# Kernel tuning notes

Hardware: AMD Instinct MI355X
Metric: run time of the kernel (lower is better)

## Reference

```python
import jax, jax.numpy as jnp
import numpy as np

D_MODEL = 512
N_HEADS = 8
D_HEAD = D_MODEL // N_HEADS
EPS = 1e-5


def layer_norm(x, g, b):
    mu = jnp.mean(x, axis=-1, keepdims=True)
    var = jnp.mean(jnp.square(x - mu), axis=-1, keepdims=True)
    return (x - mu) * jax.lax.rsqrt(var + EPS) * g + b


def setup_inputs() -> dict:
    key = jax.random.key(0)
    ks = jax.random.split(key, 8)
    B, L, D = 2, 4096, D_MODEL
    x = jax.random.normal(ks[0], (B, L, D), dtype=jnp.float32)
    # monotonically increasing event timestamps (hours)
    timestamps = jnp.sort(jax.random.uniform(ks[1], (B, L), dtype=jnp.float32) * 1000.0, axis=-1)
    mask = jnp.ones((B, L), dtype=jnp.float32)
    s = 0.02
    return {
        "x": x,
        "timestamps": timestamps,
        "mask": mask,
        "ln1_g": jnp.ones((D,), jnp.float32),
        "ln1_b": jnp.zeros((D,), jnp.float32),
        "w_qkv": jax.random.normal(ks[2], (3 * D, D), jnp.float32) * s,
        "w_out": jax.random.normal(ks[3], (D, D), jnp.float32) * s,
        "decay_rate": jnp.ones((N_HEADS,), jnp.float32) * 0.01,
        "ln2_g": jnp.ones((D,), jnp.float32),
        "ln2_b": jnp.zeros((D,), jnp.float32),
        "w_ff1": jax.random.normal(ks[4], (4 * D, D), jnp.float32) * s,
        "w_ff2": jax.random.normal(ks[5], (D, 4 * D), jnp.float32) * s,
    }


def reference(x, timestamps, mask, ln1_g, ln1_b, w_qkv, w_out, decay_rate, ln2_g, ln2_b, w_ff1, w_ff2):
    B, L, D = x.shape
    H, dh = N_HEADS, D_HEAD
    scale = dh ** (-0.5)

    xn = layer_norm(x, ln1_g, ln1_b)
    qkv = (xn @ w_qkv.T).reshape(B, L, 3, H, dh).transpose(2, 0, 3, 1, 4)  # [3,B,H,L,dh]
    q, k, v = qkv[0], qkv[1], qkv[2]

    attn = jnp.einsum("bhid,bhjd->bhij", q, k) * scale  # [B,H,L,L]

    # temporal-decay bias
    t_diff = jnp.abs(timestamps[:, None, :, None] - timestamps[:, None, None, :]) / 24.0  # [B,1,L,L]
    decay = jax.nn.softplus(decay_rate)[None, :, None, None]  # [1,H,1,1]
    attn = attn - decay * t_diff

    # causal mask
    causal = jnp.triu(jnp.ones((L, L), dtype=bool), k=1)
    attn = jnp.where(causal[None, None], -jnp.inf, attn)

    # padding mask over keys
    pad = (mask == 0)[:, None, None, :]  # [B,1,1,L]
    attn = jnp.where(pad, -jnp.inf, attn)

    attn = jax.nn.softmax(attn, axis=-1)
    out = jnp.einsum("bhij,bhjd->bhid", attn, v).transpose(0, 2, 1, 3).reshape(B, L, D)

    x = x + out @ w_out.T
    h = layer_norm(x, ln2_g, ln2_b)
    x = x + jax.nn.silu(h @ w_ff1.T) @ w_ff2.T
    return x
```

## Files before the change

### kernel.cpp

```cpp
#include <hip/hip_runtime.h>
#include <hip/hip_bf16.h>
#include <cmath>


#define L_SEQ 4096
#define D_MODEL 512
#define N_HEADS 8
#define D_HEAD 64
#define QKV_LD 1536

typedef __attribute__((ext_vector_type(8))) short bf16x8;
typedef __attribute__((ext_vector_type(4))) float f32x4;
typedef __attribute__((ext_vector_type(4))) unsigned u32x4;

__device__ __forceinline__ __hip_bfloat16 f2bf(float v) { return __float2bfloat16(v); }

__device__ __forceinline__ float exp2_raw(float x) {
  float r;
  asm("v_exp_f32 %0, %1" : "=v"(r) : "v"(x));
  return r;
}

__device__ __forceinline__ void gl_lds16(const __hip_bfloat16* g, __hip_bfloat16* l) {
  __builtin_amdgcn_global_load_lds((__attribute__((address_space(1))) void*)g,
                                   (__attribute__((address_space(3))) void*)l, 16, 0, 0);
}

__global__ __launch_bounds__(256) void cvt4b_kernel(const float* __restrict__ s0, __hip_bfloat16* __restrict__ d0,
                                                    const float* __restrict__ s1, __hip_bfloat16* __restrict__ d1,
                                                    const float* __restrict__ s2, __hip_bfloat16* __restrict__ d2,
                                                    const float* __restrict__ s3, __hip_bfloat16* __restrict__ d3,
                                                    const float* __restrict__ ts,
                                                    const float* __restrict__ mask,
                                                    const float* __restrict__ decay_rate,
                                                    float* __restrict__ biasH) {
  const int i = blockIdx.x * 256 + threadIdx.x;
  if (i < 786432) {
    const float* s;
    __hip_bfloat16* d;
    int off;
    if (i < 196608) { s = s0; d = d0; off = i; }
    else if (i < 262144) { s = s1; d = d1; off = i - 196608; }
    else if (i < 524288) { s = s2; d = d2; off = i - 262144; }
    else { s = s3; d = d3; off = i - 524288; }
    const float4 v = ((const float4*)s)[off];
    d[4 * off + 0] = f2bf(v.x);
    d[4 * off + 1] = f2bf(v.y);
    d[4 * off + 2] = f2bf(v.z);
    d[4 * off + 3] = f2bf(v.w);
  } else {
    const int idx = i - 786432;
    const int col = idx & 4095;
    const int h = (idx >> 12) & 7;
    const int b = idx >> 15;
    const float LOG2E = 1.4426950408889634f;
    const float dfac = log1pf(expf(decay_rate[h])) * (1.0f / 24.0f) * LOG2E;
    const float m = mask[b * 4096 + col];
    biasH[idx] = dfac * ts[b * 4096 + col] + (m != 0.f ? 0.f : -1e30f);
  }
}

__global__ __launch_bounds__(256) void ln_kernel(const float* __restrict__ x,
                                                 const float* __restrict__ g,
                                                 const float* __restrict__ b,
                                                 __hip_bfloat16* __restrict__ out) {
  const int row = blockIdx.x;
  const int t = threadIdx.x;
  const float* xr = x + (size_t)row * D_MODEL;
  float v0 = xr[t];
  float v1 = xr[t + 256];
  float s = v0 + v1;
  float qq = v0 * v0 + v1 * v1;
  for (int off = 32; off > 0; off >>= 1) {
    s += __shfl_xor(s, off);
    qq += __shfl_xor(qq, off);
  }
  __shared__ float red[8];
  const int wid = t >> 6;
  if ((t & 63) == 0) { red[wid] = s; red[4 + wid] = qq; }
  __syncthreads();
  s = red[0] + red[1] + red[2] + red[3];
  qq = red[4] + red[5] + red[6] + red[7];
  const float mu = s * (1.0f / 512.0f);
  const float var = fmaxf(qq * (1.0f / 512.0f) - mu * mu, 0.0f);
  const float rstd = rsqrtf(var + 1e-5f);
  __hip_bfloat16* orow = out + (size_t)row * D_MODEL;
  orow[t] = f2bf((v0 - mu) * rstd * g[t] + b[t]);
  orow[t + 256] = f2bf((v1 - mu) * rstd * g[t + 256] + b[t + 256]);
}

__global__ __launch_bounds__(256) void vtrans_kernel(const __hip_bfloat16* __restrict__ qkv,
                                                     __hip_bfloat16* __restrict__ vt) {
  const int gid = blockIdx.x * 256 + threadIdx.x;
  const int l = gid & 4095;
  const int bg = gid >> 12;
  const int b = bg >> 6, g = bg & 63;
  const int h = g >> 3, dg = (g & 7) * 8;
  const __hip_bfloat16* src = qkv + (size_t)(b * L_SEQ + l) * QKV_LD + 1024 + h * 64 + dg;
  bf16x8 v = *(const bf16x8*)src;
  const int kin = l & 63;
  const int sl = (kin & 0x23) | ((kin & 0x10) >> 2) | ((kin & 0x0c) << 1);
  const size_t dbase = (size_t)((b * 8 + h) * 64 + dg) * L_SEQ + (l & ~63) + sl;
  for (int j = 0; j < 8; j++)
    vt[dbase + (size_t)j * L_SEQ] = ((const __hip_bfloat16*)&v)[j];
}

template <int EPI>
__global__ __launch_bounds__(256) void gemm_kernel(const __hip_bfloat16* __restrict__ A,
                                                   const __hip_bfloat16* __restrict__ B,
                                                   int M, int N, int K,
                                                   const float* __restrict__ aux,
                                                   void* __restrict__ C) {
  __shared__ __align__(16) __hip_bfloat16 As[2][128 * 32];
  __shared__ __align__(16) __hip_bfloat16 Bs[2][128 * 32];
  const int tid = threadIdx.x;
  const int lane = tid & 63, w = tid >> 6;
  const int m0 = blockIdx.y * 128, n0 = blockIdx.x * 128;
  const int wm = (w >> 1) * 64, wn = (w & 1) * 64;
  const int r = lane & 15, q = lane >> 4;

  f32x4 acc[4][4];
  const f32x4 zz = {0.f, 0.f, 0.f, 0.f};
  for (int i = 0; i < 4; i++)
    for (int j = 0; j < 4; j++) acc[i][j] = zz;

  const int c0 = tid, c1 = 256 + tid;
  const int row0 = c0 >> 2, kb0 = (c0 & 3) * 8;
  const int row1 = c1 >> 2, kb1 = (c1 & 3) * 8;

#define GEMM_STAGE(k0, buf)                                                     \
  do {                                                                          \
    gl_lds16(A + (size_t)(m0 + row0) * K + ((k0) + kb0), &As[buf][c0 * 8]);     \
    gl_lds16(B + (size_t)(n0 + row0) * K + ((k0) + kb0), &Bs[buf][c0 * 8]);     \
    gl_lds16(A + (size_t)(m0 + row1) * K + ((k0) + kb1), &As[buf][c1 * 8]);     \
    gl_lds16(B + (size_t)(n0 + row1) * K + ((k0) + kb1), &Bs[buf][c1 * 8]);     \
  } while (0)

  GEMM_STAGE(0, 0);
  const int niter = K >> 5;
  for (int it = 0; it < niter; it++) {
    const int cur = it & 1;
    if (it + 1 < niter) {
      GEMM_STAGE((it + 1) << 5, cur ^ 1);
      asm volatile("s_waitcnt vmcnt(4)" ::: "memory");
    } else {
      asm volatile("s_waitcnt vmcnt(0)" ::: "memory");
    }
    __builtin_amdgcn_s_barrier();
    bf16x8 af[4], bfr[4];
    for (int mi = 0; mi < 4; mi++)
      af[mi] = *(const bf16x8*)(&As[cur][(wm + mi * 16 + r) * 32 + q * 8]);
    for (int ni = 0; ni < 4; ni++)
      bfr[ni] = *(const bf16x8*)(&Bs[cur][(wn + ni * 16 + r) * 32 + q * 8]);
    for (int mi = 0; mi < 4; mi++)
      for (int ni = 0; ni < 4; ni++)
        acc[mi][ni] = __builtin_amdgcn_mfma_f32_16x16x32_bf16(af[mi], bfr[ni], acc[mi][ni], 0, 0, 0);
    __builtin_amdgcn_s_barrier();
  }
#undef GEMM_STAGE

  for (int mi = 0; mi < 4; mi++)
    for (int ni = 0; ni < 4; ni++)
      for (int j = 0; j < 4; j++) {
        const int gm = m0 + wm + mi * 16 + q * 4 + j;
        const int gn = n0 + wn + ni * 16 + r;
        float v = acc[mi][ni][j];
        const size_t idx = (size_t)gm * N + gn;
        if (EPI == 0) {
          ((__hip_bfloat16*)C)[idx] = f2bf(v);
        } else {
          v = v / (1.0f + expf(-v));
          ((__hip_bfloat16*)C)[idx] = f2bf(v);
        }
      }
}

__global__ __launch_bounds__(256) void gemm_res64_kernel(const __hip_bfloat16* __restrict__ A,
                                                         const __hip_bfloat16* __restrict__ B,
                                                         int M, int N, int K,
                                                         const float* __restrict__ aux,
                                                         float* __restrict__ C) {
  __shared__ __align__(16) __hip_bfloat16 As[2][64 * 32];
  __shared__ __align__(16) __hip_bfloat16 Bs[2][128 * 32];
  const int tid = threadIdx.x;
  const int lane = tid & 63, w = tid >> 6;
  const int m0 = blockIdx.y * 64, n0 = blockIdx.x * 128;
  const int wm = (w >> 1) * 32, wn = (w & 1) * 64;
  const int r = lane & 15, q = lane >> 4;

  f32x4 acc[2][4];
  const f32x4 zz = {0.f, 0.f, 0.f, 0.f};
  for (int i = 0; i < 2; i++)
    for (int j = 0; j < 4; j++) acc[i][j] = zz;

  const int rowA = tid >> 2, kbA = (tid & 3) * 8;
  const int c0 = tid, c1 = 256 + tid;
  const int rowB0 = c0 >> 2, kb0 = (c0 & 3) * 8;
  const int rowB1 = c1 >> 2, kb1 = (c1 & 3) * 8;

#define GEMM_STAGE64(k0, buf)                                                    \
  do {                                                                           \
    gl_lds16(A + (size_t)(m0 + rowA) * K + ((k0) + kbA), &As[buf][tid * 8]);     \
    gl_lds16(B + (size_t)(n0 + rowB0) * K + ((k0) + kb0), &Bs[buf][c0 * 8]);     \
    gl_lds16(B + (size_t)(n0 + rowB1) * K + ((k0) + kb1), &Bs[buf][c1 * 8]);     \
  } while (0)

  GEMM_STAGE64(0, 0);
  const int niter = K >> 5;
  for (int it = 0; it < niter; it++) {
    const int cur = it & 1;
    if (it + 1 < niter) {
      GEMM_STAGE64((it + 1) << 5, cur ^ 1);
      asm volatile("s_waitcnt vmcnt(3)" ::: "memory");
    } else {
      asm volatile("s_waitcnt vmcnt(0)" ::: "memory");
    }
    __builtin_amdgcn_s_barrier();
    bf16x8 af[2], bfr[4];
    for (int mi = 0; mi < 2; mi++)
      af[mi] = *(const bf16x8*)(&As[cur][(wm + mi * 16 + r) * 32 + q * 8]);
    for (int ni = 0; ni < 4; ni++)
      bfr[ni] = *(const bf16x8*)(&Bs[cur][(wn + ni * 16 + r) * 32 + q * 8]);
    for (int mi = 0; mi < 2; mi++)
      for (int ni = 0; ni < 4; ni++)
        acc[mi][ni] = __builtin_amdgcn_mfma_f32_16x16x32_bf16(af[mi], bfr[ni], acc[mi][ni], 0, 0, 0);
    __builtin_amdgcn_s_barrier();
  }
#undef GEMM_STAGE64

  for (int mi = 0; mi < 2; mi++)
    for (int ni = 0; ni < 4; ni++)
      for (int j = 0; j < 4; j++) {
        const int gm = m0 + wm + mi * 16 + q * 4 + j;
        const int gn = n0 + wn + ni * 16 + r;
        const size_t idx = (size_t)gm * N + gn;
        C[idx] = acc[mi][ni][j] + aux[idx];
      }
}

__device__ __forceinline__ void stage_kv128(int w, int lane, int key0,
                                            const __hip_bfloat16* __restrict__ Kg,
                                            const __hip_bfloat16* __restrict__ Vg,
                                            __hip_bfloat16* Ks, __hip_bfloat16* Vs) {
  const int krow_in = lane >> 3;
  const int kcs = (lane & 7) ^ krow_in;
  const int vrow_in = lane >> 4;
  const int vch = lane & 15;
#pragma unroll
  for (int ii = 0; ii < 2; ii++) {
    const int i = w * 2 + ii;
    const int krow = i * 8 + krow_in;
    gl_lds16(Kg + (size_t)(key0 + krow) * QKV_LD + kcs * 8, Ks + i * 512 + lane * 8);
    const int vrow = i * 4 + vrow_in;
    const int vcs = vch ^ (vrow & 7);
    gl_lds16(Vg + (size_t)vrow * L_SEQ + key0 + vcs * 8, Vs + i * 512 + lane * 8);
  }
}

template <bool CAUSAL>
__device__ __forceinline__ void attn_tile128(int key0, int lw0, int r, int q,
                                             const __hip_bfloat16* Ks,
                                             const __hip_bfloat16* Vs,
                                             const float* biasLds,
                                             float scale2,
                                             const bf16x8& qf0, const bf16x8& qf1,
                                             const bf16x8& onesf,
                                             f32x4* o, f32x4& ls) {
  const int r7 = r & 7;
  const f32x4 zz = {0.f, 0.f, 0.f, 0.f};
  f32x4 bias4[8];
#pragma unroll
  for (int hc = 0; hc < 8; hc++)
    bias4[hc] = *(const f32x4*)(biasLds + key0 + hc * 16 + q * 4);
  f32x4 s[8];
  __builtin_amdgcn_s_setprio(1);
#pragma unroll
  for (int hc = 0; hc < 8; hc++) {
    const __hip_bfloat16* kr = Ks + (hc * 16 + r) * 64;
    bf16x8 k0 = *(const bf16x8*)(kr + ((q ^ r7) * 8));
    bf16x8 k1 = *(const bf16x8*)(kr + (((q + 4) ^ r7) * 8));
    f32x4 a = zz;
    a = __builtin_amdgcn_mfma_f32_16x16x32_bf16(k0, qf0, a, 0, 0, 0);
    a = __builtin_amdgcn_mfma_f32_16x16x32_bf16(k1, qf1, a, 0, 0, 0);
    s[hc] = a;
  }
  __builtin_amdgcn_s_setprio(0);
  float p[8][4];
#pragma unroll
  for (int hc = 0; hc < 8; hc++)
#pragma unroll
    for (int j = 0; j < 4; j++) {
      float pv = exp2_raw(fmaf(s[hc][j], scale2, bias4[hc][j]));
      if (CAUSAL) pv = (key0 + hc * 16 + q * 4 + j <= lw0 + r) ? pv : 0.f;
      p[hc][j] = pv;
    }
  bf16x8 pa[4];
#pragma unroll
  for (int kc = 0; kc < 4; kc++) {
    u32x4 pw;
    unsigned w0, w1, w2, w3;
    asm("v_cvt_pk_bf16_f32 %0, %1, %2" : "=v"(w0) : "v"(p[2 * kc][0]), "v"(p[2 * kc][1]));
    asm("v_cvt_pk_bf16_f32 %0, %1, %2" : "=v"(w1) : "v"(p[2 * kc][2]), "v"(p[2 * kc][3]));
    asm("v_cvt_pk_bf16_f32 %0, %1, %2" : "=v"(w2) : "v"(p[2 * kc + 1][0]), "v"(p[2 * kc + 1][1]));
    asm("v_cvt_pk_bf16_f32 %0, %1, %2" : "=v"(w3) : "v"(p[2 * kc + 1][2]), "v"(p[2 * kc + 1][3]));
    pw[0] = w0; pw[1] = w1; pw[2] = w2; pw[3] = w3;
    pa[kc] = *(bf16x8*)&pw;
  }
  __builtin_amdgcn_s_setprio(1);
#pragma unroll
  for (int kc = 0; kc < 4; kc++) {
#pragma unroll
    for (int c = 0; c < 4; c++) {
      const __hip_bfloat16* vr = Vs + (c * 16 + r) * 128 + (((kc * 4 + q) ^ r7) * 8);
      bf16x8 vf = *(const bf16x8*)vr;
      o[c] = __builtin_amdgcn_mfma_f32_16x16x32_bf16(pa[kc], vf, o[c], 0, 0, 0);
    }
    ls = __builtin_amdgcn_mfma_f32_16x16x32_bf16(pa[kc], onesf, ls, 0, 0, 0);
  }
  __builtin_amdgcn_s_setprio(0);
}

__global__ __launch_bounds__(512, 4) void attn_kernel(const __hip_bfloat16* __restrict__ qkv,
                                                      const __hip_bfloat16* __restrict__ vt,
                                                      const float* __restrict__ biasH,
                                                      __hip_bfloat16* __restrict__ out) {
  const int blk = blockIdx.x;
  const int bh = blk & 15;
  const int pr = blk >> 4;
  const int b = bh >> 3, h = bh & 7;
  const int tid = threadIdx.x, lane = tid & 63, w = tid >> 6;
  const int grp = w >> 2, wg = w & 3;
  const int qi = grp ? (63 - pr) : pr;
  const int l0 = qi * 64;
  const int lw0 = l0 + wg * 16;
  const int r = lane & 15, q = lane >> 4;

  __shared__ __align__(16) __hip_bfloat16 Ksm[2][128 * 64];
  __shared__ __align__(16) __hip_bfloat16 Vsm[2][64 * 128];
  __shared__ __align__(16) float biasLds[4096];

  const float LOG2E = 1.4426950408889634f;
  const float scale2 = 0.125f * LOG2E;

  const __hip_bfloat16* Kg = qkv + (size_t)b * L_SEQ * QKV_LD + 512 + h * 64;
  const __hip_bfloat16* Vg = vt + (size_t)bh * 64 * L_SEQ;
  const float* biasHp = biasH + (size_t)bh * L_SEQ;

  stage_kv128(w, lane, 0, Kg, Vg, Ksm[0], Vsm[0]);
#pragma unroll
  for (int ii = 0; ii < 2; ii++) {
    const int fo = (w * 2 + ii) * 256;
    gl_lds16((const __hip_bfloat16*)(biasHp + fo + lane * 4),
             (__hip_bfloat16*)(biasLds + fo + lane * 4));
  }

  bf16x8 qf0, qf1;
  {
    const __hip_bfloat16* qrow = qkv + (size_t)(b * L_SEQ + lw0 + r) * QKV_LD + h * 64 + q * 8;
    qf0 = *(const bf16x8*)qrow;
    qf1 = *(const bf16x8*)(qrow + 32);
  }

  const f32x4 zz = {0.f, 0.f, 0.f, 0.f};
  f32x4 o[4];
  for (int c = 0; c < 4; c++) o[c] = zz;
  f32x4 ls = zz;

  bf16x8 onesf;
  for (int i = 0; i < 8; i++) ((short*)&onesf)[i] = (short)0x3F80;

  const int ntA = (pr >> 1) + 1;
  const int ntB = ((63 - pr) >> 1) + 1;
  const int nt = grp ? ntB : ntA;

  for (int t = 0; t < ntB; t++) {
    const int cur = t & 1;
    if (t + 1 < ntB) {
      stage_kv128(w, lane, (t + 1) << 7, Kg, Vg, Ksm[cur ^ 1], Vsm[cur ^ 1]);
      asm volatile("s_waitcnt vmcnt(4)" ::: "memory");
    } else {
      asm volatile("s_waitcnt vmcnt(0)" ::: "memory");
    }
    __builtin_amdgcn_s_barrier();
    if (t < nt) {
      if (t == nt - 1)
        attn_tile128<true>(t << 7, lw0, r, q, Ksm[cur], Vsm[cur], biasLds, scale2, qf0, qf1,
                           onesf, o, ls);
      else
        attn_tile128<false>(t << 7, lw0, r, q, Ksm[cur], Vsm[cur], biasLds, scale2, qf0, qf1,
                            onesf, o, ls);
    }
    __builtin_amdgcn_s_barrier();
  }

  float invj[4];
  for (int j = 0; j < 4; j++) invj[j] = 1.0f / ls[j];
  for (int c = 0; c < 4; c++)
    for (int j = 0; j < 4; j++) {
      const int rowg = lw0 + q * 4 + j;
      out[(size_t)(b * L_SEQ + rowg) * D_MODEL + h * 64 + c * 16 + r] = f2bf(o[c][j] * invj[j]);
    }
}

extern "C" void kernel_launch(void* const* d_in, const int* in_sizes, int n_in,
                              void* d_out, int out_size, void* d_ws, size_t ws_size,
                              hipStream_t stream) {
  const float* x = (const float*)d_in[0];
  const float* ts = (const float*)d_in[1];
  const float* mask = (const float*)d_in[2];
  const float* ln1_g = (const float*)d_in[3];
  const float* ln1_b = (const float*)d_in[4];
  const float* w_qkv = (const float*)d_in[5];
  const float* w_out = (const float*)d_in[6];
  const float* decay = (const float*)d_in[7];
  const float* ln2_g = (const float*)d_in[8];
  const float* ln2_b = (const float*)d_in[9];
  const float* w_ff1 = (const float*)d_in[10];
  const float* w_ff2 = (const float*)d_in[11];

  char* ws = (char*)d_ws;
  __hip_bfloat16* wqkv_b = (__hip_bfloat16*)(ws + 0);
  __hip_bfloat16* wout_b = (__hip_bfloat16*)(ws + 1572864);
  __hip_bfloat16* wff1_b = (__hip_bfloat16*)(ws + 2097152);
  __hip_bfloat16* wff2_b = (__hip_bfloat16*)(ws + 4194304);
  __hip_bfloat16* xn = (__hip_bfloat16*)(ws + 6291456);
  __hip_bfloat16* vt = (__hip_bfloat16*)(ws + 6291456);
  __hip_bfloat16* qkv = (__hip_bfloat16*)(ws + 14680064);
  __hip_bfloat16* attnout = (__hip_bfloat16*)(ws + 39845888);
  __hip_bfloat16* h = attnout;
  __hip_bfloat16* ff1out = (__hip_bfloat16*)(ws + 6291456);
  float* x2 = (float*)(ws + 48234496);
  float* biasH = (float*)(ws + 48234496);
  float* out = (float*)d_out;

  const int M = 2 * L_SEQ;

  cvt4b_kernel<<<dim3(3328), dim3(256), 0, stream>>>(w_qkv, wqkv_b, w_out, wout_b,
                                                     w_ff1, wff1_b, w_ff2, wff2_b,
                                                     ts, mask, decay, biasH);

  ln_kernel<<<dim3(M), dim3(256), 0, stream>>>(x, ln1_g, ln1_b, xn);
  gemm_kernel<0><<<dim3(12, 64), dim3(256), 0, stream>>>(xn, wqkv_b, M, 1536, 512, nullptr, qkv);
  vtrans_kernel<<<dim3(2048), dim3(256), 0, stream>>>(qkv, vt);
  attn_kernel<<<dim3(512), dim3(512), 0, stream>>>(qkv, vt, biasH, attnout);
  gemm_res64_kernel<<<dim3(4, 128), dim3(256), 0, stream>>>(attnout, wout_b, M, 512, 512, x, x2);
  ln_kernel<<<dim3(M), dim3(256), 0, stream>>>(x2, ln2_g, ln2_b, h);
  gemm_kernel<2><<<dim3(16, 64), dim3(256), 0, stream>>>(h, wff1_b, M, 2048, 512, nullptr, ff1out);
  gemm_res64_kernel<<<dim3(4, 128), dim3(256), 0, stream>>>(ff1out, wff2_b, M, 512, 2048, x2, out);
}
```

Before: 268.0 us.

## Restructure attention blocks to two waves processing paired query tiles sequentially

The attention kernel drops from 8 waves per block to 2. Each wave now handles 32 query rows as two 16-row halves, so every K/V fragment read from LDS feeds two sets of MFMAs. Each block runs its two paired query tiles (j and 63-j) one after the other instead of concurrently. This is meant to increase register-level reuse of K/V and cut idle waves that previously waited on barriers, at the cost of fewer waves to hide latency, a heavier per-wave staging load, and a one-tile prefetch wasted at the phase boundary.

Result: slower. 295.0 us (+10.1%).

```diff
diff --git a/kernel.cpp b/kernel.cpp
--- a/kernel.cpp
+++ b/kernel.cpp
@@ -238,17 +238,17 @@
       }
 }
 
-__device__ __forceinline__ void stage_kv128(int w, int lane, int key0,
-                                            const __hip_bfloat16* __restrict__ Kg,
-                                            const __hip_bfloat16* __restrict__ Vg,
-                                            __hip_bfloat16* Ks, __hip_bfloat16* Vs) {
+__device__ __forceinline__ void stage_kv128_w2(int w, int lane, int key0,
+                                               const __hip_bfloat16* __restrict__ Kg,
+                                               const __hip_bfloat16* __restrict__ Vg,
+                                               __hip_bfloat16* Ks, __hip_bfloat16* Vs) {
   const int krow_in = lane >> 3;
   const int kcs = (lane & 7) ^ krow_in;
   const int vrow_in = lane >> 4;
   const int vch = lane & 15;
 #pragma unroll
-  for (int ii = 0; ii < 2; ii++) {
-    const int i = w * 2 + ii;
+  for (int ii = 0; ii < 8; ii++) {
+    const int i = w * 8 + ii;
     const int krow = i * 8 + krow_in;
     gl_lds16(Kg + (size_t)(key0 + krow) * QKV_LD + kcs * 8, Ks + i * 512 + lane * 8);
     const int vrow = i * 4 + vrow_in;
@@ -258,53 +258,67 @@
 }
 
 template <bool CAUSAL>
-__device__ __forceinline__ void attn_tile128(int key0, int lw0, int r, int q,
-                                             const __hip_bfloat16* Ks,
-                                             const __hip_bfloat16* Vs,
-                                             const float* biasLds,
-                                             float scale2,
-                                             const bf16x8& qf0, const bf16x8& qf1,
-                                             const bf16x8& onesf,
-                                             f32x4* o, f32x4& ls) {
+__device__ __forceinline__ void attn_tile128d(int key0, int lw0a, int r, int q,
+                                              const __hip_bfloat16* Ks,
+                                              const __hip_bfloat16* Vs,
+                                              const float* biasLds, float scale2,
+                                              const bf16x8& qfa0, const bf16x8& qfa1,
+                                              const bf16x8& qfb0, const bf16x8& qfb1,
+                                              const bf16x8& onesf,
+                                              f32x4* oa, f32x4* ob, f32x4& lsa, f32x4& lsb) {
   const int r7 = r & 7;
   const f32x4 zz = {0.f, 0.f, 0.f, 0.f};
   f32x4 bias4[8];
 #pragma unroll
   for (int hc = 0; hc < 8; hc++)
     bias4[hc] = *(const f32x4*)(biasLds + key0 + hc * 16 + q * 4);
-  f32x4 s[8];
+  f32x4 sa[8], sb[8];
   __builtin_amdgcn_s_setprio(1);
 #pragma unroll
   for (int hc = 0; hc < 8; hc++) {
     const __hip_bfloat16* kr = Ks + (hc * 16 + r) * 64;
     bf16x8 k0 = *(const bf16x8*)(kr + ((q ^ r7) * 8));
     bf16x8 k1 = *(const bf16x8*)(kr + (((q + 4) ^ r7) * 8));
-    f32x4 a = zz;
-    a = __builtin_amdgcn_mfma_f32_16x16x32_bf16(k0, qf0, a, 0, 0, 0);
-    a = __builtin_amdgcn_mfma_f32_16x16x32_bf16(k1, qf1, a, 0, 0, 0);
-    s[hc] = a;
+    f32x4 a = __builtin_amdgcn_mfma_f32_16x16x32_bf16(k0, qfa0, zz, 0, 0, 0);
+    a = __builtin_amdgcn_mfma_f32_16x16x32_bf16(k1, qfa1, a, 0, 0, 0);
+    sa[hc] = a;
+    f32x4 bb = __builtin_amdgcn_mfma_f32_16x16x32_bf16(k0, qfb0, zz, 0, 0, 0);
+    bb = __builtin_amdgcn_mfma_f32_16x16x32_bf16(k1, qfb1, bb, 0, 0, 0);
+    sb[hc] = bb;
   }
   __builtin_amdgcn_s_setprio(0);
-  float p[8][4];
+  float pa_[8][4], pb_[8][4];
 #pragma unroll
   for (int hc = 0; hc < 8; hc++)
 #pragma unroll
     for (int j = 0; j < 4; j++) {
-      float pv = exp2_raw(fmaf(s[hc][j], scale2, bias4[hc][j]));
-      if (CAUSAL) pv = (key0 + hc * 16 + q * 4 + j <= lw0 + r) ? pv : 0.f;
-      p[hc][j] = pv;
+      const int key = key0 + hc * 16 + q * 4 + j;
+      float pva = exp2_raw(fmaf(sa[hc][j], scale2, bias4[hc][j]));
+      float pvb = exp2_raw(fmaf(sb[hc][j], scale2, bias4[hc][j]));
+      if (CAUSAL) {
+        pva = (key <= lw0a + r) ? pva : 0.f;
+        pvb = (key <= lw0a + 16 + r) ? pvb : 0.f;
+      }
+      pa_[hc][j] = pva;
+      pb_[hc][j] = pvb;
     }
-  bf16x8 pa[4];
+  bf16x8 paa[4], pab[4];
 #pragma unroll
   for (int kc = 0; kc < 4; kc++) {
     u32x4 pw;
     unsigned w0, w1, w2, w3;
-    asm("v_cvt_pk_bf16_f32 %0, %1, %2" : "=v"(w0) : "v"(p[2 * kc][0]), "v"(p[2 * kc][1]));
-    asm("v_cvt_pk_bf16_f32 %0, %1, %2" : "=v"(w1) : "v"(p[2 * kc][2]), "v"(p[2 * kc][3]));
-    asm("v_cvt_pk_bf16_f32 %0, %1, %2" : "=v"(w2) : "v"(p[2 * kc + 1][0]), "v"(p[2 * kc + 1][1]));
-    asm("v_cvt_pk_bf16_f32 %0, %1, %2" : "=v"(w3) : "v"(p[2 * kc + 1][2]), "v"(p[2 * kc + 1][3]));
+    asm("v_cvt_pk_bf16_f32 %0, %1, %2" : "=v"(w0) : "v"(pa_[2 * kc][0]), "v"(pa_[2 * kc][1]));
+    asm("v_cvt_pk_bf16_f32 %0, %1, %2" : "=v"(w1) : "v"(pa_[2 * kc][2]), "v"(pa_[2 * kc][3]));
+    asm("v_cvt_pk_bf16_f32 %0, %1, %2" : "=v"(w2) : "v"(pa_[2 * kc + 1][0]), "v"(pa_[2 * kc + 1][1]));
+    asm("v_cvt_pk_bf16_f32 %0, %1, %2" : "=v"(w3) : "v"(pa_[2 * kc + 1][2]), "v"(pa_[2 * kc + 1][3]));
     pw[0] = w0; pw[1] = w1; pw[2] = w2; pw[3] = w3;
-    pa[kc] = *(bf16x8*)&pw;
+    paa[kc] = *(bf16x8*)&pw;
+    asm("v_cvt_pk_bf16_f32 %0, %1, %2" : "=v"(w0) : "v"(pb_[2 * kc][0]), "v"(pb_[2 * kc][1]));
+    asm("v_cvt_pk_bf16_f32 %0, %1, %2" : "=v"(w1) : "v"(pb_[2 * kc][2]), "v"(pb_[2 * kc][3]));
+    asm("v_cvt_pk_bf16_f32 %0, %1, %2" : "=v"(w2) : "v"(pb_[2 * kc + 1][0]), "v"(pb_[2 * kc + 1][1]));
+    asm("v_cvt_pk_bf16_f32 %0, %1, %2" : "=v"(w3) : "v"(pb_[2 * kc + 1][2]), "v"(pb_[2 * kc + 1][3]));
+    pw[0] = w0; pw[1] = w1; pw[2] = w2; pw[3] = w3;
+    pab[kc] = *(bf16x8*)&pw;
   }
   __builtin_amdgcn_s_setprio(1);
 #pragma unroll
@@ -313,27 +327,30 @@
     for (int c = 0; c < 4; c++) {
       const __hip_bfloat16* vr = Vs + (c * 16 + r) * 128 + (((kc * 4 + q) ^ r7) * 8);
       bf16x8 vf = *(const bf16x8*)vr;
-      o[c] = __builtin_amdgcn_mfma_f32_16x16x32_bf16(pa[kc], vf, o[c], 0, 0, 0);
+      oa[c] = __builtin_amdgcn_mfma_f32_16x16x32_bf16(paa[kc], vf, oa[c], 0, 0, 0);
+      ob[c] = __builtin_amdgcn_mfma_f32_16x16x32_bf16(pab[kc], vf, ob[c], 0, 0, 0);
     }
-    ls = __builtin_amdgcn_mfma_f32_16x16x32_bf16(pa[kc], onesf, ls, 0, 0, 0);
+    lsa = __builtin_amdgcn_mfma_f32_16x16x32_bf16(paa[kc], onesf, lsa, 0, 0, 0);
+    lsb = __builtin_amdgcn_mfma_f32_16x16x32_bf16(pab[kc], onesf, lsb, 0, 0, 0);
   }
   __builtin_amdgcn_s_setprio(0);
 }
 
-__global__ __launch_bounds__(512, 4) void attn_kernel(const __hip_bfloat16* __restrict__ qkv,
+__global__ __launch_bounds__(128, 1) void attn_kernel(const __hip_bfloat16* __restrict__ qkv,
                                                       const __hip_bfloat16* __restrict__ vt,
                                                       const float* __restrict__ biasH,
                                                       __hip_bfloat16* __restrict__ out) {
   const int blk = blockIdx.x;
   const int bh = blk & 15;
-  const int pr = blk >> 4;
+  const int j = blk >> 4;
   const int b = bh >> 3, h = bh & 7;
   const int tid = threadIdx.x, lane = tid & 63, w = tid >> 6;
-  const int grp = w >> 2, wg = w & 3;
-  const int qi = grp ? (63 - pr) : pr;
-  const int l0 = qi * 64;
-  const int lw0 = l0 + wg * 16;
   const int r = lane & 15, q = lane >> 4;
+
+  const int qi1 = j, qi2 = 63 - j;
+  const int nt1 = (qi1 >> 1) + 1, nt2 = (qi2 >> 1) + 1;
+  const int lwa1 = qi1 * 64 + w * 32;
+  const int lwa2 = qi2 * 64 + w * 32;
 
   __shared__ __align__(16) __hip_bfloat16 Ksm[2][128 * 64];
   __shared__ __align__(16) __hip_bfloat16 Vsm[2][64 * 128];
@@ -346,60 +363,94 @@
   const __hip_bfloat16* Vg = vt + (size_t)bh * 64 * L_SEQ;
   const float* biasHp = biasH + (size_t)bh * L_SEQ;
 
-  stage_kv128(w, lane, 0, Kg, Vg, Ksm[0], Vsm[0]);
-#pragma unroll
-  for (int ii = 0; ii < 2; ii++) {
-    const int fo = (w * 2 + ii) * 256;
+  stage_kv128_w2(w, lane, 0, Kg, Vg, Ksm[0], Vsm[0]);
+#pragma unroll
+  for (int ii = 0; ii < 8; ii++) {
+    const int fo = (w * 8 + ii) * 256;
     gl_lds16((const __hip_bfloat16*)(biasHp + fo + lane * 4),
              (__hip_bfloat16*)(biasLds + fo + lane * 4));
   }
 
-  bf16x8 qf0, qf1;
+  bf16x8 qfa0, qfa1, qfb0, qfb1;
   {
-    const __hip_bfloat16* qrow = qkv + (size_t)(b * L_SEQ + lw0 + r) * QKV_LD + h * 64 + q * 8;
-    qf0 = *(const bf16x8*)qrow;
-    qf1 = *(const bf16x8*)(qrow + 32);
+    const __hip_bfloat16* qa = qkv + (size_t)(b * L_SEQ + lwa1 + r) * QKV_LD + h * 64 + q * 8;
+    qfa0 = *(const bf16x8*)qa;
+    qfa1 = *(const bf16x8*)(qa + 32);
+    const __hip_bfloat16* qb = qa + (size_t)16 * QKV_LD;
+    qfb0 = *(const bf16x8*)qb;
+    qfb1 = *(const bf16x8*)(qb + 32);
   }
 
   const f32x4 zz = {0.f, 0.f, 0.f, 0.f};
-  f32x4 o[4];
-  for (int c = 0; c < 4; c++) o[c] = zz;
-  f32x4 ls = zz;
+  f32x4 oa[4], ob[4];
+  for (int c = 0; c < 4; c++) { oa[c] = zz; ob[c] = zz; }
+  f32x4 lsa = zz, lsb = zz;
 
   bf16x8 onesf;
   for (int i = 0; i < 8; i++) ((short*)&onesf)[i] = (short)0x3F80;
 
-  const int ntA = (pr >> 1) + 1;
-  const int ntB = ((63 - pr) >> 1) + 1;
-  const int nt = grp ? ntB : ntA;
-
-  for (int t = 0; t < ntB; t++) {
+  for (int t = 0; t < nt1; t++) {
     const int cur = t & 1;
-    if (t + 1 < ntB) {
-      stage_kv128(w, lane, (t + 1) << 7, Kg, Vg, Ksm[cur ^ 1], Vsm[cur ^ 1]);
-      asm volatile("s_waitcnt vmcnt(4)" ::: "memory");
+    const int nk = (t + 1 < nt1) ? (t + 1) : 0;
+    stage_kv128_w2(w, lane, nk << 7, Kg, Vg, Ksm[cur ^ 1], Vsm[cur ^ 1]);
+    asm volatile("s_waitcnt vmcnt(16)" ::: "memory");
+    __builtin_amdgcn_s_barrier();
+    if (t == nt1 - 1)
+      attn_tile128d<true>(t << 7, lwa1, r, q, Ksm[cur], Vsm[cur], biasLds, scale2,
+                          qfa0, qfa1, qfb0, qfb1, onesf, oa, ob, lsa, lsb);
+    else
+      attn_tile128d<false>(t << 7, lwa1, r, q, Ksm[cur], Vsm[cur], biasLds, scale2,
+                           qfa0, qfa1, qfb0, qfb1, onesf, oa, ob, lsa, lsb);
+    __builtin_amdgcn_s_barrier();
+  }
+
+  {
+    float ija[4], ijb[4];
+    for (int jj = 0; jj < 4; jj++) { ija[jj] = 1.0f / lsa[jj]; ijb[jj] = 1.0f / lsb[jj]; }
+    for (int c = 0; c < 4; c++)
+      for (int jj = 0; jj < 4; jj++) {
+        const int ra = lwa1 + q * 4 + jj;
+        out[(size_t)(b * L_SEQ + ra) * D_MODEL + h * 64 + c * 16 + r] = f2bf(oa[c][jj] * ija[jj]);
+        out[(size_t)(b * L_SEQ + ra + 16) * D_MODEL + h * 64 + c * 16 + r] = f2bf(ob[c][jj] * ijb[jj]);
+      }
+    for (int c = 0; c < 4; c++) { oa[c] = zz; ob[c] = zz; }
+    lsa = zz; lsb = zz;
+    const __hip_bfloat16* qa = qkv + (size_t)(b * L_SEQ + lwa2 + r) * QKV_LD + h * 64 + q * 8;
+    qfa0 = *(const bf16x8*)qa;
+    qfa1 = *(const bf16x8*)(qa + 32);
+    const __hip_bfloat16* qb = qa + (size_t)16 * QKV_LD;
+    qfb0 = *(const bf16x8*)qb;
+    qfb1 = *(const bf16x8*)(qb + 32);
+  }
+
+  for (int t = 0; t < nt2; t++) {
+    const int cur = (nt1 + t) & 1;
+    if (t + 1 < nt2) {
+      stage_kv128_w2(w, lane, (t + 1) << 7, Kg, Vg, Ksm[cur ^ 1], Vsm[cur ^ 1]);
+      asm volatile("s_waitcnt vmcnt(16)" ::: "memory");
     } else {
       asm volatile("s_waitcnt vmcnt(0)" ::: "memory");
     }
     __builtin_amdgcn_s_barrier();
-    if (t < nt) {
-      if (t == nt - 1)
-        attn_tile128<true>(t << 7, lw0, r, q, Ksm[cur], Vsm[cur], biasLds, scale2, qf0, qf1,
-                           onesf, o, ls);
-      else
-        attn_tile128<false>(t << 7, lw0, r, q, Ksm[cur], Vsm[cur], biasLds, scale2, qf0, qf1,
-                            onesf, o, ls);
-    }
-    __builtin_amdgcn_s_barrier();
-  }
-
-  float invj[4];
-  for (int j = 0; j < 4; j++) invj[j] = 1.0f / ls[j];
-  for (int c = 0; c < 4; c++)
-    for (int j = 0; j < 4; j++) {
-      const int rowg = lw0 + q * 4 + j;
-      out[(size_t)(b * L_SEQ + rowg) * D_MODEL + h * 64 + c * 16 + r] = f2bf(o[c][j] * invj[j]);
-    }
+    if (t == nt2 - 1)
+      attn_tile128d<true>(t << 7, lwa2, r, q, Ksm[cur], Vsm[cur], biasLds, scale2,
+                          qfa0, qfa1, qfb0, qfb1, onesf, oa, ob, lsa, lsb);
+    else
+      attn_tile128d<false>(t << 7, lwa2, r, q, Ksm[cur], Vsm[cur], biasLds, scale2,
+                           qfa0, qfa1, qfb0, qfb1, onesf, oa, ob, lsa, lsb);
+    __builtin_amdgcn_s_barrier();
+  }
+
+  {
+    float ija[4], ijb[4];
+    for (int jj = 0; jj < 4; jj++) { ija[jj] = 1.0f / lsa[jj]; ijb[jj] = 1.0f / lsb[jj]; }
+    for (int c = 0; c < 4; c++)
+      for (int jj = 0; jj < 4; jj++) {
+        const int ra = lwa2 + q * 4 + jj;
+        out[(size_t)(b * L_SEQ + ra) * D_MODEL + h * 64 + c * 16 + r] = f2bf(oa[c][jj] * ija[jj]);
+        out[(size_t)(b * L_SEQ + ra + 16) * D_MODEL + h * 64 + c * 16 + r] = f2bf(ob[c][jj] * ijb[jj]);
+      }
+  }
 }
 
 extern "C" void kernel_launch(void* const* d_in, const int* in_sizes, int n_in,
@@ -442,7 +493,7 @@
   ln_kernel<<<dim3(M), dim3(256), 0, stream>>>(x, ln1_g, ln1_b, xn);
   gemm_kernel<0><<<dim3(12, 64), dim3(256), 0, stream>>>(xn, wqkv_b, M, 1536, 512, nullptr, qkv);
   vtrans_kernel<<<dim3(2048), dim3(256), 0, stream>>>(qkv, vt);
-  attn_kernel<<<dim3(512), dim3(512), 0, stream>>>(qkv, vt, biasH, attnout);
+  attn_kernel<<<dim3(512), dim3(128), 0, stream>>>(qkv, vt, biasH, attnout);
   gemm_res64_kernel<<<dim3(4, 128), dim3(256), 0, stream>>>(attnout, wout_b, M, 512, 512, x, x2);
   ln_kernel<<<dim3(M), dim3(256), 0, stream>>>(x2, ln2_g, ln2_b, h);
   gemm_kernel<2><<<dim3(16, 64), dim3(256), 0, stream>>>(h, wff1_b, M, 2048, 512, nullptr, ff1out);
```
